# Performance work log

Hardware: AMD Instinct MI355X
Metric: run time of the kernel (lower is better)

The kernel has to match this reference:

```python
import jax, jax.numpy as jnp
import numpy as np

DIM = 192
HEADS = 4


def setup_inputs() -> dict:
    key = jax.random.key(0)
    ks = jax.random.split(key, 6)
    b, h, w = 8, 128, 128
    return {
        "x": jax.random.normal(ks[0], (b, DIM, h, w), jnp.float32),
        "svp_fea": jax.random.normal(ks[1], (b, 3, h, w), jnp.float32),
        "qkv_w": jax.random.normal(ks[2], (3 * DIM, DIM), jnp.float32) * 0.02,
        "dw_w": jax.random.normal(ks[3], (3 * DIM, 1, 3, 3), jnp.float32) * 0.02,
        "svp_w": jax.random.normal(ks[4], (3 * HEADS, 3), jnp.float32) * 0.02,
        "proj_w": jax.random.normal(ks[5], (DIM, DIM + 3 * HEADS), jnp.float32) * 0.02,
        "temperature": jnp.ones((HEADS, 1, 1), jnp.float32),
    }


def _l2norm(t):
    # F.normalize(t, dim=-1): divide by max(||t||_2, eps)
    return t / jnp.maximum(jnp.linalg.norm(t, axis=-1, keepdims=True), 1e-12)


def reference(x, svp_fea, qkv_w, dw_w, svp_w, proj_w, temperature):
    b, c, h, w = x.shape
    heads = temperature.shape[0]
    # 1x1 conv (dim -> 3*dim), then 3x3 depthwise conv (groups = 3*dim)
    qkv = jnp.einsum('bchw,oc->bohw', x, qkv_w)
    qkv = jax.lax.conv_general_dilated(
        qkv, dw_w, window_strides=(1, 1), padding=((1, 1), (1, 1)),
        dimension_numbers=('NCHW', 'OIHW', 'NCHW'), feature_group_count=3 * c)
    # 1x1 conv on illumination prior: 3 -> 3*heads
    svp_q = jnp.einsum('bchw,oc->bohw', svp_fea, svp_w)
    q, k, v = jnp.split(qkv, 3, axis=1)
    ch = c // heads
    hw = h * w
    q = _l2norm(q.reshape(b, heads, ch, hw))
    k = _l2norm(k.reshape(b, heads, ch, hw))
    v = v.reshape(b, heads, ch, hw)
    sq = _l2norm(svp_q.reshape(b, heads, 3, hw))
    q = jnp.concatenate([q, sq], axis=2)            # [b, head, ch+3, hw]
    logits = jnp.einsum('bhcn,bhdn->bhcd', q, k) * temperature[None]
    attn = jax.nn.softmax(logits, axis=-1)          # softmax over channel dim d
    out = jnp.einsum('bhcd,bhdn->bhcn', attn, v)    # [b, head, ch+3, hw]
    out = out.reshape(b, heads * (ch + 3), h, w)
    return jnp.einsum('bchw,oc->bohw', out, proj_w)
```

## Files before the change

### kernel.cpp

```cpp
#include <hip/hip_runtime.h>
#include <hip/hip_bf16.h>
#include <math.h>

#define BB   8
#define CCH  192
#define OCN  576
#define HWD  128
#define HWN  16384
#define NH   4
#define CHD  48
#define C51  51
#define GSZ  (C51*48)

typedef __hip_bfloat16 bf16;
typedef __attribute__((ext_vector_type(8))) short short8;
typedef __attribute__((ext_vector_type(4))) float f32x4;

__device__ __forceinline__ float bfbits2f(unsigned int u16) {
  union { unsigned int i; float f; } v; v.i = u16 << 16; return v.f;
}
__device__ __forceinline__ unsigned short f2bfbits(float f) {
  __hip_bfloat16 h = __float2bfloat16(f);
  return *(unsigned short*)&h;
}
__device__ __forceinline__ void stage16(const void* g, void* l) {
  __builtin_amdgcn_global_load_lds(
      (const __attribute__((address_space(1))) void*)g,
      (__attribute__((address_space(3))) void*)l, 16, 0, 0);
}

__global__ __launch_bounds__(256) void k_svp(
    const float* __restrict__ svp_fea, const float* __restrict__ svp_w,
    float* __restrict__ svp_q, float* __restrict__ ssq_svp_p)
{
  __shared__ float lsw[4][12];
  const int b = blockIdx.y;
  const int t = threadIdx.x;
  const int n = blockIdx.x * 256 + t;
  const int wave = t >> 6;
  const float* fb = svp_fea + (size_t)b * 3 * HWN;
  const float f0 = fb[n], f1 = fb[HWN + n], f2 = fb[2 * HWN + n];
  float* ob = svp_q + (size_t)b * 12 * HWN + n;
  #pragma unroll
  for (int r = 0; r < 12; ++r) {
    float o = svp_w[r*3]*f0 + svp_w[r*3+1]*f1 + svp_w[r*3+2]*f2;
    ob[(size_t)r * HWN] = o;
    float v = o * o;
    #pragma unroll
    for (int off = 32; off >= 1; off >>= 1) v += __shfl_down(v, off, 64);
    if ((t & 63) == 0) lsw[wave][r] = v;
  }
  __syncthreads();
  if (t < 12) {
    float s = lsw[0][t] + lsw[1][t] + lsw[2][t] + lsw[3][t];
    ssq_svp_p[((size_t)b * 12 + t) * 64 + blockIdx.x] = s;
  }
}

__global__ __launch_bounds__(256) void k_castw(
    const float* __restrict__ w, unsigned short* __restrict__ wb)
{
  const int i = (blockIdx.x * 256 + threadIdx.x) * 4;
  float4 v = *(const float4*)(w + i);
  union { uint2 u; unsigned short s[4]; } pk;
  pk.s[0] = f2bfbits(v.x); pk.s[1] = f2bfbits(v.y);
  pk.s[2] = f2bfbits(v.z); pk.s[3] = f2bfbits(v.w);
  *(uint2*)(wb + i) = pk.u;
}

__global__ __launch_bounds__(256) void k_gemm(
    const float* __restrict__ x, const unsigned short* __restrict__ wb,
    unsigned short* __restrict__ qkv1)
{
  __shared__ unsigned short Xs[64 * CCH];
  __shared__ unsigned short Ws[96 * CCH];
  const int b = blockIdx.y;
  const int n0 = blockIdx.x * 64;
  const int t = threadIdx.x;
  const int lane = t & 63, wave = t >> 6;
  const int wm = wave >> 1, wn = wave & 1;
  const int lq = lane >> 4, lr = lane & 15;

  const float* xb = x + (size_t)b * CCH * HWN + n0;
  #pragma unroll
  for (int rr = 0; rr < 6; ++rr) {
    int idx = rr * 256 + t;
    int cp = idx >> 4, nq = idx & 15;
    int c0 = cp * 2;
    float4 v0 = *(const float4*)(xb + (size_t)c0 * HWN + nq * 4);
    float4 v1 = *(const float4*)(xb + (size_t)(c0 + 1) * HWN + nq * 4);
    int g = c0 >> 3, co = c0 & 7;
    float a0[4] = {v0.x, v0.y, v0.z, v0.w};
    float a1[4] = {v1.x, v1.y, v1.z, v1.w};
    #pragma unroll
    for (int j = 0; j < 4; ++j) {
      int n = nq * 4 + j;
      int gs = (g & ~7) | ((g & 7) ^ (n & 7) ^ ((n >> 3) & 7));
      unsigned int pk = (unsigned int)f2bfbits(a0[j])
                      | ((unsigned int)f2bfbits(a1[j]) << 16);
      *(unsigned int*)&Xs[n * CCH + gs * 8 + co] = pk;
    }
  }

  for (int mc = 0; mc < 6; ++mc) {
    const unsigned short* wsrc = wb + (size_t)mc * 96 * CCH;
    #pragma unroll
    for (int i = 0; i < 9; ++i) {
      int chunk = wave * 9 + i;
      int d = chunk * 64 + lane;
      int row = d / 24, kg = d % 24;
      int skg = (kg & ~7) | ((kg & 7) ^ (row & 7));
      stage16(wsrc + (size_t)row * CCH + skg * 8, &Ws[0] + chunk * 512);
    }
    asm volatile("s_waitcnt vmcnt(0)" ::: "memory");
    __syncthreads();

    f32x4 acc[3][2];
    #pragma unroll
    for (int mf = 0; mf < 3; ++mf)
      #pragma unroll
      for (int nf = 0; nf < 2; ++nf) acc[mf][nf] = (f32x4)0.f;

    #pragma unroll
    for (int ks = 0; ks < 6; ++ks) {
      const int gk = ks * 4 + lq;
      short8 a[3], bb[2];
      #pragma unroll
      for (int mf = 0; mf < 3; ++mf) {
        int r = wm * 48 + mf * 16 + lr;
        int sg = (gk & ~7) | ((gk & 7) ^ (r & 7));
        a[mf] = *(const short8*)&Ws[r * CCH + sg * 8];
      }
      #pragma unroll
      for (int nf = 0; nf < 2; ++nf) {
        int r = wn * 32 + nf * 16 + lr;
        int sg = (gk & ~7) | ((gk & 7) ^ (r & 7) ^ ((r >> 3) & 7));
        bb[nf] = *(const short8*)&Xs[r * CCH + sg * 8];
      }
      #pragma unroll
      for (int mf = 0; mf < 3; ++mf)
        #pragma unroll
        for (int nf = 0; nf < 2; ++nf)
          acc[mf][nf] = __builtin_amdgcn_mfma_f32_16x16x32_bf16(
              a[mf], bb[nf], acc[mf][nf], 0, 0, 0);
    }

    unsigned short* ob = qkv1 + ((size_t)b * OCN + mc * 96 + wm * 48) * HWN
                         + n0 + wn * 32;
    #pragma unroll
    for (int mf = 0; mf < 3; ++mf)
      #pragma unroll
      for (int nf = 0; nf < 2; ++nf)
        #pragma unroll
        for (int r = 0; r < 4; ++r) {
          int m = mf * 16 + lq * 4 + r;
          int n = nf * 16 + lr;
          ob[(size_t)m * HWN + n] = f2bfbits(acc[mf][nf][r]);
        }
    __syncthreads();
  }
}

__global__ __launch_bounds__(256) void k_dw(
    const unsigned short* __restrict__ qkv1, const float* __restrict__ dw_w,
    unsigned short* __restrict__ qkv, float* __restrict__ ssq_qk_p)
{
  __shared__ float lsw[4];
  const int b = blockIdx.z, c = blockIdx.y, slab = blockIdx.x;
  const int t = threadIdx.x;
  const int cg = t & 15, rg = t >> 4;
  const int y0 = slab * 32 + rg * 2;
  const unsigned short* src = qkv1 + ((size_t)b * OCN + c) * HWN;
  float w[9];
  #pragma unroll
  for (int i = 0; i < 9; ++i) w[i] = dw_w[c * 9 + i];

  float rows[4][10];
  #pragma unroll
  for (int j = 0; j < 4; ++j) {
    int gr = y0 - 1 + j;
    uint4 B = make_uint4(0u, 0u, 0u, 0u);
    unsigned int Al = 0; unsigned int Cv = 0;
    if ((unsigned)gr < 128u) {
      const unsigned short* rp = src + (size_t)gr * HWD;
      B = *(const uint4*)(rp + cg * 8);
      if (cg > 0)  Al = *(const unsigned int*)(rp + cg * 8 - 2);
      if (cg < 15) Cv = (unsigned int)rp[cg * 8 + 8];
    }
    rows[j][0] = bfbits2f(Al >> 16);
    unsigned int ub[4] = {B.x, B.y, B.z, B.w};
    #pragma unroll
    for (int q = 0; q < 4; ++q) {
      rows[j][1 + 2*q] = bfbits2f(ub[q] & 0xffffu);
      rows[j][2 + 2*q] = bfbits2f(ub[q] >> 16);
    }
    rows[j][9] = bfbits2f(Cv);
  }

  unsigned short* dst = qkv + ((size_t)b * OCN + c) * HWN;
  float ssq = 0.f;
  #pragma unroll
  for (int e = 0; e < 2; ++e) {
    float acc[8];
    #pragma unroll
    for (int i = 0; i < 8; ++i) acc[i] = 0.f;
    #pragma unroll
    for (int j = 0; j < 3; ++j) {
      const float* vr = rows[e + j];
      #pragma unroll
      for (int i = 0; i < 8; ++i)
        acc[i] += w[j*3]*vr[i] + w[j*3+1]*vr[i+1] + w[j*3+2]*vr[i+2];
    }
    union { uint4 u; unsigned short s[8]; } pk;
    #pragma unroll
    for (int i = 0; i < 8; ++i) pk.s[i] = f2bfbits(acc[i]);
    *(uint4*)(dst + (size_t)(y0 + e) * HWD + cg * 8) = pk.u;
    if (c < 384) {
      #pragma unroll
      for (int i = 0; i < 8; ++i) {
        float rv = bfbits2f(pk.s[i]);
        ssq += rv * rv;
      }
    }
  }
  if (c < 384) {
    #pragma unroll
    for (int off = 32; off >= 1; off >>= 1) ssq += __shfl_down(ssq, off, 64);
    if ((t & 63) == 0) lsw[t >> 6] = ssq;
  }
  __syncthreads();
  if (c < 384 && t == 0)
    ssq_qk_p[(((size_t)b * 384 + c) << 2) | slab] =
        lsw[0] + lsw[1] + lsw[2] + lsw[3];
}

__global__ __launch_bounds__(256) void k_gram(
    const unsigned short* __restrict__ qkv, const float* __restrict__ svp_q,
    float* __restrict__ Gp)
{
  __shared__ float Gs[C51 * 50];
  const int chunk = blockIdx.x, h = blockIdx.y, b = blockIdx.z;
  const int t = threadIdx.x;
  const int lane = t & 63, wave = t >> 6;
  const int lq = lane >> 4, lr = lane & 15;
  const unsigned short* qb = qkv + ((size_t)b*OCN + h*CHD)*HWN;
  const unsigned short* kb = qkv + ((size_t)b*OCN + 192 + h*CHD)*HWN;
  const float* sb = svp_q + ((size_t)b*12 + h*3)*HWN;

  for (int idx = t; idx < C51*50; idx += 256) Gs[idx] = 0.f;

  f32x4 acc[3][3], sacc[3];
  #pragma unroll
  for (int mf = 0; mf < 3; ++mf)
    #pragma unroll
    for (int nf = 0; nf < 3; ++nf) acc[mf][nf] = (f32x4)0.f;
  #pragma unroll
  for (int nf = 0; nf < 3; ++nf) sacc[nf] = (f32x4)0.f;

  const int nbase = chunk * 1024 + wave * 256;
  #pragma unroll 4
  for (int ks = 0; ks < 8; ++ks) {
    const int n = nbase + ks * 32 + lq * 8;
    short8 a[3], bb[3];
    #pragma unroll
    for (int mf = 0; mf < 3; ++mf)
      a[mf] = *(const short8*)&qb[(size_t)(mf*16 + lr)*HWN + n];
    #pragma unroll
    for (int nf = 0; nf < 3; ++nf)
      bb[nf] = *(const short8*)&kb[(size_t)(nf*16 + lr)*HWN + n];
    union { short8 s8; unsigned short us[8]; } sv;
    #pragma unroll
    for (int i = 0; i < 8; ++i) sv.us[i] = 0;
    if (lr < 3) {
      const float* sp = sb + (size_t)lr*HWN + n;
      float4 v0 = *(const float4*)sp, v1 = *(const float4*)(sp + 4);
      sv.us[0] = f2bfbits(v0.x); sv.us[1] = f2bfbits(v0.y);
      sv.us[2] = f2bfbits(v0.z); sv.us[3] = f2bfbits(v0.w);
      sv.us[4] = f2bfbits(v1.x); sv.us[5] = f2bfbits(v1.y);
      sv.us[6] = f2bfbits(v1.z); sv.us[7] = f2bfbits(v1.w);
    }
    #pragma unroll
    for (int mf = 0; mf < 3; ++mf)
      #pragma unroll
      for (int nf = 0; nf < 3; ++nf)
        acc[mf][nf] = __builtin_amdgcn_mfma_f32_16x16x32_bf16(
            a[mf], bb[nf], acc[mf][nf], 0, 0, 0);
    #pragma unroll
    for (int nf = 0; nf < 3; ++nf)
      sacc[nf] = __builtin_amdgcn_mfma_f32_16x16x32_bf16(
          sv.s8, bb[nf], sacc[nf], 0, 0, 0);
  }

  __syncthreads();
  for (int w = 0; w < 4; ++w) {
    if (wave == w) {
      #pragma unroll
      for (int mf = 0; mf < 3; ++mf)
        #pragma unroll
        for (int nf = 0; nf < 3; ++nf)
          #pragma unroll
          for (int r = 0; r < 4; ++r)
            Gs[(mf*16 + lq*4 + r)*50 + nf*16 + lr] += acc[mf][nf][r];
      if (lq == 0) {
        #pragma unroll
        for (int nf = 0; nf < 3; ++nf)
          #pragma unroll
          for (int r = 0; r < 3; ++r)
            Gs[(48 + r)*50 + nf*16 + lr] += sacc[nf][r];
      }
    }
    __syncthreads();
  }
  float* Gout = Gp + ((size_t)((b*NH + h) * 16 + chunk)) * GSZ;
  for (int idx = t; idx < GSZ; idx += 256) {
    int row = idx / 48, col = idx - row * 48;
    Gout[idx] = Gs[row*50 + col];
  }
}

__global__ __launch_bounds__(256) void k_attn_fold(
    const float* __restrict__ Gp, const float* __restrict__ ssq_qk_p,
    const float* __restrict__ ssq_svp_p, const float* __restrict__ temperature,
    const float* __restrict__ proj_w, unsigned short* __restrict__ W2bf)
{
  __shared__ float A[GSZ];
  __shared__ float qinv[C51];
  __shared__ float kinv[48];
  const int h = blockIdx.x, b = blockIdx.y;
  const int t = threadIdx.x;
  const float* Gb = Gp + ((size_t)(b*NH + h) * 16) * GSZ;
  if (t < 48) {
    const float* p = ssq_qk_p + (((size_t)b * 384 + 192 + h*48 + t) << 2);
    kinv[t] = 1.f / fmaxf(sqrtf(p[0] + p[1] + p[2] + p[3]), 1e-12f);
  }
  if (t >= 64 && t < 64 + C51) {
    int c = t - 64;
    float ss;
    if (c < 48) {
      const float* p = ssq_qk_p + (((size_t)b * 384 + h*48 + c) << 2);
      ss = p[0] + p[1] + p[2] + p[3];
    } else {
      const float* p = ssq_svp_p + ((size_t)b * 12 + h*3 + (c - 48)) * 64;
      float s0 = 0.f, s1 = 0.f, s2 = 0.f, s3 = 0.f;
      #pragma unroll
      for (int i = 0; i < 16; ++i) {
        float4 v = *(const float4*)(p + i * 4);
        s0 += v.x; s1 += v.y; s2 += v.z; s3 += v.w;
      }
      ss = (s0 + s1) + (s2 + s3);
    }
    qinv[c] = 1.f / fmaxf(sqrtf(ss), 1e-12f);
  }
  for (int idx = t; idx < GSZ; idx += 256) {
    float s = 0.f;
    #pragma unroll
    for (int c = 0; c < 16; ++c) s += Gb[(size_t)c * GSZ + idx];
    A[idx] = s;
  }
  __syncthreads();
  const float temp = temperature[h];
  if (t < C51) {
    float row[48];
    float m = -1e30f;
    const float qi = qinv[t] * temp;
    #pragma unroll
    for (int d = 0; d < 48; ++d) {
      float l = A[t*48 + d] * qi * kinv[d];
      row[d] = l; m = fmaxf(m, l);
    }
    float s = 0.f;
    #pragma unroll
    for (int d = 0; d < 48; ++d) { row[d] = expf(row[d] - m); s += row[d]; }
    const float inv = 1.f / s;
    #pragma unroll
    for (int d = 0; d < 48; ++d) A[t*48 + d] = row[d] * inv;
  }
  __syncthreads();
  for (int idx = t; idx < 192*48; idx += 256) {
    int o = idx / 48, d = idx - o*48;
    const float* pw = proj_w + o*204 + C51*h;
    float s = 0.f;
    #pragma unroll
    for (int c = 0; c < C51; ++c) s += pw[c] * A[c*48 + d];
    W2bf[((size_t)b*CCH + o)*CCH + h*48 + d] = f2bfbits(s);
  }
}

__global__ __launch_bounds__(256) void k_out(
    const unsigned short* __restrict__ qkv, const unsigned short* __restrict__ w2b,
    float* __restrict__ out)
{
  __shared__ unsigned short Vs[64 * CCH];
  __shared__ unsigned short Ws[96 * CCH];
  const int b = blockIdx.y;
  const int n0 = blockIdx.x * 64;
  const int t = threadIdx.x;
  const int lane = t & 63, wave = t >> 6;
  const int wm = wave >> 1, wn = wave & 1;
  const int lq = lane >> 4, lr = lane & 15;

  const unsigned short* vb = qkv + ((size_t)b * OCN + 384) * HWN + n0;
  #pragma unroll
  for (int rr = 0; rr < 3; ++rr) {
    int idx = rr * 256 + t;
    int cp = idx >> 3, nq = idx & 7;
    int c0 = cp * 2;
    uint4 v0 = *(const uint4*)(vb + (size_t)c0 * HWN + nq * 8);
    uint4 v1 = *(const uint4*)(vb + (size_t)(c0 + 1) * HWN + nq * 8);
    union { uint4 u; unsigned short s[8]; } p0, p1;
    p0.u = v0; p1.u = v1;
    int g = c0 >> 3, co = c0 & 7;
    #pragma unroll
    for (int j = 0; j < 8; ++j) {
      int n = nq * 8 + j;
      int gs = (g & ~7) | ((g & 7) ^ (n & 7) ^ ((n >> 3) & 7));
      unsigned int pk = (unsigned int)p0.s[j] | ((unsigned int)p1.s[j] << 16);
      *(unsigned int*)&Vs[n * CCH + gs * 8 + co] = pk;
    }
  }

  for (int mc = 0; mc < 2; ++mc) {
    const unsigned short* wsrc = w2b + ((size_t)b * CCH + mc * 96) * CCH;
    #pragma unroll
    for (int i = 0; i < 9; ++i) {
      int chunk = wave * 9 + i;
      int d = chunk * 64 + lane;
      int row = d / 24, kg = d % 24;
      int skg = (kg & ~7) | ((kg & 7) ^ (row & 7));
      stage16(wsrc + (size_t)row * CCH + skg * 8, &Ws[0] + chunk * 512);
    }
    asm volatile("s_waitcnt vmcnt(0)" ::: "memory");
    __syncthreads();

    f32x4 acc[3][2];
    #pragma unroll
    for (int mf = 0; mf < 3; ++mf)
      #pragma unroll
      for (int nf = 0; nf < 2; ++nf) acc[mf][nf] = (f32x4)0.f;

    #pragma unroll
    for (int ks = 0; ks < 6; ++ks) {
      const int gk = ks * 4 + lq;
      short8 a[3], bb[2];
      #pragma unroll
      for (int mf = 0; mf < 3; ++mf) {
        int r = wm * 48 + mf * 16 + lr;
        int sg = (gk & ~7) | ((gk & 7) ^ (r & 7));
        a[mf] = *(const short8*)&Ws[r * CCH + sg * 8];
      }
      #pragma unroll
      for (int nf = 0; nf < 2; ++nf) {
        int r = wn * 32 + nf * 16 + lr;
        int sg = (gk & ~7) | ((gk & 7) ^ (r & 7) ^ ((r >> 3) & 7));
        bb[nf] = *(const short8*)&Vs[r * CCH + sg * 8];
      }
      #pragma unroll
      for (int mf = 0; mf < 3; ++mf)
        #pragma unroll
        for (int nf = 0; nf < 2; ++nf)
          acc[mf][nf] = __builtin_amdgcn_mfma_f32_16x16x32_bf16(
              a[mf], bb[nf], acc[mf][nf], 0, 0, 0);
    }

    float* ob = out + ((size_t)b * CCH + mc * 96 + wm * 48) * HWN + n0 + wn * 32;
    #pragma unroll
    for (int mf = 0; mf < 3; ++mf)
      #pragma unroll
      for (int nf = 0; nf < 2; ++nf)
        #pragma unroll
        for (int r = 0; r < 4; ++r) {
          int m = mf * 16 + lq * 4 + r;
          int n = nf * 16 + lr;
          ob[(size_t)m * HWN + n] = acc[mf][nf][r];
        }
    __syncthreads();
  }
}

extern "C" void kernel_launch(void* const* d_in, const int* in_sizes, int n_in,
                              void* d_out, int out_size, void* d_ws, size_t ws_size,
                              hipStream_t stream)
{
  const float* x       = (const float*)d_in[0];
  const float* svp_fea = (const float*)d_in[1];
  const float* qkv_w   = (const float*)d_in[2];
  const float* dw_w    = (const float*)d_in[3];
  const float* svp_w   = (const float*)d_in[4];
  const float* proj_w  = (const float*)d_in[5];
  const float* temp    = (const float*)d_in[6];
  float* outp = (float*)d_out;

  char* ws = (char*)d_ws;
  const size_t off_qkv1   = 0;
  const size_t off_qkv    = off_qkv1  + (size_t)BB*OCN*HWN*2;
  const size_t off_wb     = off_qkv   + (size_t)BB*OCN*HWN*2;
  const size_t off_svpq   = off_wb    + (size_t)OCN*CCH*2;
  const size_t off_ssqqk  = off_svpq  + (size_t)BB*12*HWN*4;
  const size_t off_ssqsvp = off_ssqqk + (size_t)BB*384*4*4;
  const size_t off_Gp     = off_ssqsvp+ (size_t)BB*12*64*4;
  const size_t off_W2     = off_Gp    + (size_t)BB*NH*16*GSZ*4;

  unsigned short* qkv1  = (unsigned short*)(ws + off_qkv1);
  bf16*  qkv     = (bf16*)(ws + off_qkv);
  unsigned short* wb    = (unsigned short*)(ws + off_wb);
  float* svp_q   = (float*)(ws + off_svpq);
  float* ssq_qk_p  = (float*)(ws + off_ssqqk);
  float* ssq_svp_p = (float*)(ws + off_ssqsvp);
  float* Gp      = (float*)(ws + off_Gp);
  unsigned short* W2bf  = (unsigned short*)(ws + off_W2);

  k_castw    <<<dim3(108),         256, 0, stream>>>(qkv_w, wb);
  k_svp      <<<dim3(64, BB),      256, 0, stream>>>(svp_fea, svp_w, svp_q, ssq_svp_p);
  k_gemm     <<<dim3(256, BB),     256, 0, stream>>>(x, wb, qkv1);
  k_dw       <<<dim3(4, OCN, BB),  256, 0, stream>>>(qkv1, dw_w, (unsigned short*)qkv, ssq_qk_p);
  k_gram     <<<dim3(16, NH, BB),  256, 0, stream>>>((const unsigned short*)qkv, svp_q, Gp);
  k_attn_fold<<<dim3(NH, BB),      256, 0, stream>>>(Gp, ssq_qk_p, ssq_svp_p, temp, proj_w, W2bf);
  k_out      <<<dim3(256, BB),     256, 0, stream>>>((const unsigned short*)qkv, W2bf, outp);
}
```

Before: 282.7 us.

## Load weight fragments directly from global into registers and hoist B fragments

In both the qkv GEMM and the output GEMM, the weight tile is no longer staged through LDS with global_load_lds. Each wave now reads its A fragments straight from global memory into registers. The activation fragments are read from LDS once into registers before the output-channel loop, which removes the per-iteration barriers and LDS traffic and halves LDS use per block, so occupancy can rise. In exchange, weight rows are re-read from global or L2 by every wave with less coalescing, and register pressure goes up from holding 18 A and 12 B fragments.

```diff
diff --git a/kernel.cpp b/kernel.cpp
--- a/kernel.cpp
+++ b/kernel.cpp
@@ -23,11 +23,6 @@
   __hip_bfloat16 h = __float2bfloat16(f);
   return *(unsigned short*)&h;
 }
-__device__ __forceinline__ void stage16(const void* g, void* l) {
-  __builtin_amdgcn_global_load_lds(
-      (const __attribute__((address_space(1))) void*)g,
-      (__attribute__((address_space(3))) void*)l, 16, 0, 0);
-}
 
 __global__ __launch_bounds__(256) void k_svp(
     const float* __restrict__ svp_fea, const float* __restrict__ svp_w,
@@ -73,7 +68,6 @@
     unsigned short* __restrict__ qkv1)
 {
   __shared__ unsigned short Xs[64 * CCH];
-  __shared__ unsigned short Ws[96 * CCH];
   const int b = blockIdx.y;
   const int n0 = blockIdx.x * 64;
   const int t = threadIdx.x;
@@ -101,20 +95,29 @@
       *(unsigned int*)&Xs[n * CCH + gs * 8 + co] = pk;
     }
   }
+  __syncthreads();
+
+  short8 bfr[2][6];
+  #pragma unroll
+  for (int nf = 0; nf < 2; ++nf) {
+    int r = wn * 32 + nf * 16 + lr;
+    #pragma unroll
+    for (int ks = 0; ks < 6; ++ks) {
+      int gk = ks * 4 + lq;
+      int sg = (gk & ~7) | ((gk & 7) ^ (r & 7) ^ ((r >> 3) & 7));
+      bfr[nf][ks] = *(const short8*)&Xs[r * CCH + sg * 8];
+    }
+  }
 
   for (int mc = 0; mc < 6; ++mc) {
-    const unsigned short* wsrc = wb + (size_t)mc * 96 * CCH;
-    #pragma unroll
-    for (int i = 0; i < 9; ++i) {
-      int chunk = wave * 9 + i;
-      int d = chunk * 64 + lane;
-      int row = d / 24, kg = d % 24;
-      int skg = (kg & ~7) | ((kg & 7) ^ (row & 7));
-      stage16(wsrc + (size_t)row * CCH + skg * 8, &Ws[0] + chunk * 512);
-    }
-    asm volatile("s_waitcnt vmcnt(0)" ::: "memory");
-    __syncthreads();
-
+    const unsigned short* wsrc = wb + ((size_t)mc * 96 + wm * 48 + lr) * CCH;
+    short8 a[3][6];
+    #pragma unroll
+    for (int mf = 0; mf < 3; ++mf)
+      #pragma unroll
+      for (int ks = 0; ks < 6; ++ks)
+        a[mf][ks] = *(const short8*)(wsrc + (size_t)mf * 16 * CCH
+                                     + (ks * 4 + lq) * 8);
     f32x4 acc[3][2];
     #pragma unroll
     for (int mf = 0; mf < 3; ++mf)
@@ -122,28 +125,13 @@
       for (int nf = 0; nf < 2; ++nf) acc[mf][nf] = (f32x4)0.f;
 
     #pragma unroll
-    for (int ks = 0; ks < 6; ++ks) {
-      const int gk = ks * 4 + lq;
-      short8 a[3], bb[2];
-      #pragma unroll
-      for (int mf = 0; mf < 3; ++mf) {
-        int r = wm * 48 + mf * 16 + lr;
-        int sg = (gk & ~7) | ((gk & 7) ^ (r & 7));
-        a[mf] = *(const short8*)&Ws[r * CCH + sg * 8];
-      }
-      #pragma unroll
-      for (int nf = 0; nf < 2; ++nf) {
-        int r = wn * 32 + nf * 16 + lr;
-        int sg = (gk & ~7) | ((gk & 7) ^ (r & 7) ^ ((r >> 3) & 7));
-        bb[nf] = *(const short8*)&Xs[r * CCH + sg * 8];
-      }
+    for (int ks = 0; ks < 6; ++ks)
       #pragma unroll
       for (int mf = 0; mf < 3; ++mf)
         #pragma unroll
         for (int nf = 0; nf < 2; ++nf)
           acc[mf][nf] = __builtin_amdgcn_mfma_f32_16x16x32_bf16(
-              a[mf], bb[nf], acc[mf][nf], 0, 0, 0);
-    }
+              a[mf][ks], bfr[nf][ks], acc[mf][nf], 0, 0, 0);
 
     unsigned short* ob = qkv1 + ((size_t)b * OCN + mc * 96 + wm * 48) * HWN
                          + n0 + wn * 32;
@@ -157,7 +145,6 @@
           int n = nf * 16 + lr;
           ob[(size_t)m * HWN + n] = f2bfbits(acc[mf][nf][r]);
         }
-    __syncthreads();
   }
 }
 
@@ -391,7 +378,6 @@
     float* __restrict__ out)
 {
   __shared__ unsigned short Vs[64 * CCH];
-  __shared__ unsigned short Ws[96 * CCH];
   const int b = blockIdx.y;
   const int n0 = blockIdx.x * 64;
   const int t = threadIdx.x;
@@ -418,20 +404,29 @@
       *(unsigned int*)&Vs[n * CCH + gs * 8 + co] = pk;
     }
   }
+  __syncthreads();
+
+  short8 bfr[2][6];
+  #pragma unroll
+  for (int nf = 0; nf < 2; ++nf) {
+    int r = wn * 32 + nf * 16 + lr;
+    #pragma unroll
+    for (int ks = 0; ks < 6; ++ks) {
+      int gk = ks * 4 + lq;
+      int sg = (gk & ~7) | ((gk & 7) ^ (r & 7) ^ ((r >> 3) & 7));
+      bfr[nf][ks] = *(const short8*)&Vs[r * CCH + sg * 8];
+    }
+  }
 
   for (int mc = 0; mc < 2; ++mc) {
-    const unsigned short* wsrc = w2b + ((size_t)b * CCH + mc * 96) * CCH;
-    #pragma unroll
-    for (int i = 0; i < 9; ++i) {
-      int chunk = wave * 9 + i;
-      int d = chunk * 64 + lane;
-      int row = d / 24, kg = d % 24;
-      int skg = (kg & ~7) | ((kg & 7) ^ (row & 7));
-      stage16(wsrc + (size_t)row * CCH + skg * 8, &Ws[0] + chunk * 512);
-    }
-    asm volatile("s_waitcnt vmcnt(0)" ::: "memory");
-    __syncthreads();
-
+    const unsigned short* wsrc = w2b + ((size_t)b * CCH + mc * 96 + wm * 48 + lr) * CCH;
+    short8 a[3][6];
+    #pragma unroll
+    for (int mf = 0; mf < 3; ++mf)
+      #pragma unroll
+      for (int ks = 0; ks < 6; ++ks)
+        a[mf][ks] = *(const short8*)(wsrc + (size_t)mf * 16 * CCH
+                                     + (ks * 4 + lq) * 8);
     f32x4 acc[3][2];
     #pragma unroll
     for (int mf = 0; mf < 3; ++mf)
@@ -439,28 +434,13 @@
       for (int nf = 0; nf < 2; ++nf) acc[mf][nf] = (f32x4)0.f;
 
     #pragma unroll
-    for (int ks = 0; ks < 6; ++ks) {
-      const int gk = ks * 4 + lq;
-      short8 a[3], bb[2];
-      #pragma unroll
-      for (int mf = 0; mf < 3; ++mf) {
-        int r = wm * 48 + mf * 16 + lr;
-        int sg = (gk & ~7) | ((gk & 7) ^ (r & 7));
-        a[mf] = *(const short8*)&Ws[r * CCH + sg * 8];
-      }
-      #pragma unroll
-      for (int nf = 0; nf < 2; ++nf) {
-        int r = wn * 32 + nf * 16 + lr;
-        int sg = (gk & ~7) | ((gk & 7) ^ (r & 7) ^ ((r >> 3) & 7));
-        bb[nf] = *(const short8*)&Vs[r * CCH + sg * 8];
-      }
+    for (int ks = 0; ks < 6; ++ks)
       #pragma unroll
       for (int mf = 0; mf < 3; ++mf)
         #pragma unroll
         for (int nf = 0; nf < 2; ++nf)
           acc[mf][nf] = __builtin_amdgcn_mfma_f32_16x16x32_bf16(
-              a[mf], bb[nf], acc[mf][nf], 0, 0, 0);
-    }
+              a[mf][ks], bfr[nf][ks], acc[mf][nf], 0, 0, 0);
 
     float* ob = out + ((size_t)b * CCH + mc * 96 + wm * 48) * HWN + n0 + wn * 32;
     #pragma unroll
@@ -473,7 +453,6 @@
           int n = nf * 16 + lr;
           ob[(size_t)m * HWN + n] = acc[mf][nf][r];
         }
-    __syncthreads();
   }
 }
 
```

After: 362.4 us. 1.28x slower.

## Double-buffer weight tiles and keep B fragments in registers in GEMM kernels

Applied to the files above, without the earlier changes.

Both the qkv 1x1-conv GEMM and the output projection GEMM now stream the weight matrix in 32-row chunks through a two-slot LDS buffer. The next chunk is prefetched while the current one is multiplied, and the input (X or V) MFMA fragments are loaded from LDS into registers once instead of on every chunk. The aim is to hide global weight-load latency behind MFMA work, cut repeated LDS reads, and lower LDS footprint so more blocks fit per CU. In exchange there are more loop iterations and barriers, and each wave issues fewer MFMAs per chunk, which may limit instruction-level parallelism.

```diff
diff --git a/kernel.cpp b/kernel.cpp
--- a/kernel.cpp
+++ b/kernel.cpp
@@ -73,13 +73,22 @@
     unsigned short* __restrict__ qkv1)
 {
   __shared__ unsigned short Xs[64 * CCH];
-  __shared__ unsigned short Ws[96 * CCH];
+  __shared__ unsigned short Wd[2][32 * CCH];
   const int b = blockIdx.y;
   const int n0 = blockIdx.x * 64;
   const int t = threadIdx.x;
   const int lane = t & 63, wave = t >> 6;
   const int wm = wave >> 1, wn = wave & 1;
   const int lq = lane >> 4, lr = lane & 15;
+
+  #pragma unroll
+  for (int i = 0; i < 3; ++i) {
+    int chunk = wave * 3 + i;
+    int d = chunk * 64 + lane;
+    int row = d / 24, kg = d % 24;
+    int skg = (kg & ~7) | ((kg & 7) ^ (row & 7));
+    stage16(wb + (size_t)row * CCH + skg * 8, &Wd[0][0] + chunk * 512);
+  }
 
   const float* xb = x + (size_t)b * CCH * HWN + n0;
   #pragma unroll
@@ -101,63 +110,60 @@
       *(unsigned int*)&Xs[n * CCH + gs * 8 + co] = pk;
     }
   }
-
-  for (int mc = 0; mc < 6; ++mc) {
-    const unsigned short* wsrc = wb + (size_t)mc * 96 * CCH;
-    #pragma unroll
-    for (int i = 0; i < 9; ++i) {
-      int chunk = wave * 9 + i;
-      int d = chunk * 64 + lane;
-      int row = d / 24, kg = d % 24;
-      int skg = (kg & ~7) | ((kg & 7) ^ (row & 7));
-      stage16(wsrc + (size_t)row * CCH + skg * 8, &Ws[0] + chunk * 512);
-    }
-    asm volatile("s_waitcnt vmcnt(0)" ::: "memory");
-    __syncthreads();
-
-    f32x4 acc[3][2];
-    #pragma unroll
-    for (int mf = 0; mf < 3; ++mf)
-      #pragma unroll
-      for (int nf = 0; nf < 2; ++nf) acc[mf][nf] = (f32x4)0.f;
-
+  __syncthreads();
+
+  short8 bfr[2][6];
+  #pragma unroll
+  for (int nf = 0; nf < 2; ++nf) {
+    int r = wn * 32 + nf * 16 + lr;
+    #pragma unroll
+    for (int ks = 0; ks < 6; ++ks) {
+      int gk = ks * 4 + lq;
+      int sg = (gk & ~7) | ((gk & 7) ^ (r & 7) ^ ((r >> 3) & 7));
+      bfr[nf][ks] = *(const short8*)&Xs[r * CCH + sg * 8];
+    }
+  }
+
+  for (int mc = 0; mc < 18; ++mc) {
+    if (mc + 1 < 18) {
+      const unsigned short* wsrc = wb + (size_t)(mc + 1) * 32 * CCH;
+      unsigned short* nb = &Wd[(mc + 1) & 1][0];
+      #pragma unroll
+      for (int i = 0; i < 3; ++i) {
+        int chunk = wave * 3 + i;
+        int d = chunk * 64 + lane;
+        int row = d / 24, kg = d % 24;
+        int skg = (kg & ~7) | ((kg & 7) ^ (row & 7));
+        stage16(wsrc + (size_t)row * CCH + skg * 8, nb + chunk * 512);
+      }
+      asm volatile("s_waitcnt vmcnt(3)" ::: "memory");
+    } else {
+      asm volatile("s_waitcnt vmcnt(0)" ::: "memory");
+    }
+    __builtin_amdgcn_s_barrier();
+    asm volatile("" ::: "memory");
+
+    const unsigned short* wbuf = &Wd[mc & 1][0];
+    f32x4 acc0 = (f32x4)0.f, acc1 = (f32x4)0.f;
     #pragma unroll
     for (int ks = 0; ks < 6; ++ks) {
       const int gk = ks * 4 + lq;
-      short8 a[3], bb[2];
-      #pragma unroll
-      for (int mf = 0; mf < 3; ++mf) {
-        int r = wm * 48 + mf * 16 + lr;
-        int sg = (gk & ~7) | ((gk & 7) ^ (r & 7));
-        a[mf] = *(const short8*)&Ws[r * CCH + sg * 8];
-      }
-      #pragma unroll
-      for (int nf = 0; nf < 2; ++nf) {
-        int r = wn * 32 + nf * 16 + lr;
-        int sg = (gk & ~7) | ((gk & 7) ^ (r & 7) ^ ((r >> 3) & 7));
-        bb[nf] = *(const short8*)&Xs[r * CCH + sg * 8];
-      }
-      #pragma unroll
-      for (int mf = 0; mf < 3; ++mf)
-        #pragma unroll
-        for (int nf = 0; nf < 2; ++nf)
-          acc[mf][nf] = __builtin_amdgcn_mfma_f32_16x16x32_bf16(
-              a[mf], bb[nf], acc[mf][nf], 0, 0, 0);
-    }
-
-    unsigned short* ob = qkv1 + ((size_t)b * OCN + mc * 96 + wm * 48) * HWN
+      int r = wm * 16 + lr;
+      int sg = (gk & ~7) | ((gk & 7) ^ (r & 7));
+      short8 a = *(const short8*)&wbuf[r * CCH + sg * 8];
+      acc0 = __builtin_amdgcn_mfma_f32_16x16x32_bf16(a, bfr[0][ks], acc0, 0, 0, 0);
+      acc1 = __builtin_amdgcn_mfma_f32_16x16x32_bf16(a, bfr[1][ks], acc1, 0, 0, 0);
+    }
+
+    unsigned short* ob = qkv1 + ((size_t)b * OCN + mc * 32 + wm * 16) * HWN
                          + n0 + wn * 32;
     #pragma unroll
-    for (int mf = 0; mf < 3; ++mf)
-      #pragma unroll
-      for (int nf = 0; nf < 2; ++nf)
-        #pragma unroll
-        for (int r = 0; r < 4; ++r) {
-          int m = mf * 16 + lq * 4 + r;
-          int n = nf * 16 + lr;
-          ob[(size_t)m * HWN + n] = f2bfbits(acc[mf][nf][r]);
-        }
-    __syncthreads();
+    for (int r = 0; r < 4; ++r) {
+      ob[(size_t)(lq * 4 + r) * HWN + lr]      = f2bfbits(acc0[r]);
+      ob[(size_t)(lq * 4 + r) * HWN + 16 + lr] = f2bfbits(acc1[r]);
+    }
+    asm volatile("" ::: "memory");
+    __builtin_amdgcn_s_barrier();
   }
 }
 
@@ -391,13 +397,23 @@
     float* __restrict__ out)
 {
   __shared__ unsigned short Vs[64 * CCH];
-  __shared__ unsigned short Ws[96 * CCH];
+  __shared__ unsigned short Wd[2][32 * CCH];
   const int b = blockIdx.y;
   const int n0 = blockIdx.x * 64;
   const int t = threadIdx.x;
   const int lane = t & 63, wave = t >> 6;
   const int wm = wave >> 1, wn = wave & 1;
   const int lq = lane >> 4, lr = lane & 15;
+
+  const unsigned short* w2base = w2b + (size_t)b * CCH * CCH;
+  #pragma unroll
+  for (int i = 0; i < 3; ++i) {
+    int chunk = wave * 3 + i;
+    int d = chunk * 64 + lane;
+    int row = d / 24, kg = d % 24;
+    int skg = (kg & ~7) | ((kg & 7) ^ (row & 7));
+    stage16(w2base + (size_t)row * CCH + skg * 8, &Wd[0][0] + chunk * 512);
+  }
 
   const unsigned short* vb = qkv + ((size_t)b * OCN + 384) * HWN + n0;
   #pragma unroll
@@ -418,62 +434,59 @@
       *(unsigned int*)&Vs[n * CCH + gs * 8 + co] = pk;
     }
   }
-
-  for (int mc = 0; mc < 2; ++mc) {
-    const unsigned short* wsrc = w2b + ((size_t)b * CCH + mc * 96) * CCH;
-    #pragma unroll
-    for (int i = 0; i < 9; ++i) {
-      int chunk = wave * 9 + i;
-      int d = chunk * 64 + lane;
-      int row = d / 24, kg = d % 24;
-      int skg = (kg & ~7) | ((kg & 7) ^ (row & 7));
-      stage16(wsrc + (size_t)row * CCH + skg * 8, &Ws[0] + chunk * 512);
-    }
-    asm volatile("s_waitcnt vmcnt(0)" ::: "memory");
-    __syncthreads();
-
-    f32x4 acc[3][2];
-    #pragma unroll
-    for (int mf = 0; mf < 3; ++mf)
-      #pragma unroll
-      for (int nf = 0; nf < 2; ++nf) acc[mf][nf] = (f32x4)0.f;
-
+  __syncthreads();
+
+  short8 bfr[2][6];
+  #pragma unroll
+  for (int nf = 0; nf < 2; ++nf) {
+    int r = wn * 32 + nf * 16 + lr;
+    #pragma unroll
+    for (int ks = 0; ks < 6; ++ks) {
+      int gk = ks * 4 + lq;
+      int sg = (gk & ~7) | ((gk & 7) ^ (r & 7) ^ ((r >> 3) & 7));
+      bfr[nf][ks] = *(const short8*)&Vs[r * CCH + sg * 8];
+    }
+  }
+
+  for (int mc = 0; mc < 6; ++mc) {
+    if (mc + 1 < 6) {
+      const unsigned short* wsrc = w2base + (size_t)(mc + 1) * 32 * CCH;
+      unsigned short* nb = &Wd[(mc + 1) & 1][0];
+      #pragma unroll
+      for (int i = 0; i < 3; ++i) {
+        int chunk = wave * 3 + i;
+        int d = chunk * 64 + lane;
+        int row = d / 24, kg = d % 24;
+        int skg = (kg & ~7) | ((kg & 7) ^ (row & 7));
+        stage16(wsrc + (size_t)row * CCH + skg * 8, nb + chunk * 512);
+      }
+      asm volatile("s_waitcnt vmcnt(3)" ::: "memory");
+    } else {
+      asm volatile("s_waitcnt vmcnt(0)" ::: "memory");
+    }
+    __builtin_amdgcn_s_barrier();
+    asm volatile("" ::: "memory");
+
+    const unsigned short* wbuf = &Wd[mc & 1][0];
+    f32x4 acc0 = (f32x4)0.f, acc1 = (f32x4)0.f;
     #pragma unroll
     for (int ks = 0; ks < 6; ++ks) {
       const int gk = ks * 4 + lq;
-      short8 a[3], bb[2];
-      #pragma unroll
-      for (int mf = 0; mf < 3; ++mf) {
-        int r = wm * 48 + mf * 16 + lr;
-        int sg = (gk & ~7) | ((gk & 7) ^ (r & 7));
-        a[mf] = *(const short8*)&Ws[r * CCH + sg * 8];
-      }
-      #pragma unroll
-      for (int nf = 0; nf < 2; ++nf) {
-        int r = wn * 32 + nf * 16 + lr;
-        int sg = (gk & ~7) | ((gk & 7) ^ (r & 7) ^ ((r >> 3) & 7));
-        bb[nf] = *(const short8*)&Vs[r * CCH + sg * 8];
-      }
-      #pragma unroll
-      for (int mf = 0; mf < 3; ++mf)
-        #pragma unroll
-        for (int nf = 0; nf < 2; ++nf)
-          acc[mf][nf] = __builtin_amdgcn_mfma_f32_16x16x32_bf16(
-              a[mf], bb[nf], acc[mf][nf], 0, 0, 0);
-    }
-
-    float* ob = out + ((size_t)b * CCH + mc * 96 + wm * 48) * HWN + n0 + wn * 32;
-    #pragma unroll
-    for (int mf = 0; mf < 3; ++mf)
-      #pragma unroll
-      for (int nf = 0; nf < 2; ++nf)
-        #pragma unroll
-        for (int r = 0; r < 4; ++r) {
-          int m = mf * 16 + lq * 4 + r;
-          int n = nf * 16 + lr;
-          ob[(size_t)m * HWN + n] = acc[mf][nf][r];
-        }
-    __syncthreads();
+      int r = wm * 16 + lr;
+      int sg = (gk & ~7) | ((gk & 7) ^ (r & 7));
+      short8 a = *(const short8*)&wbuf[r * CCH + sg * 8];
+      acc0 = __builtin_amdgcn_mfma_f32_16x16x32_bf16(a, bfr[0][ks], acc0, 0, 0, 0);
+      acc1 = __builtin_amdgcn_mfma_f32_16x16x32_bf16(a, bfr[1][ks], acc1, 0, 0, 0);
+    }
+
+    float* ob = out + ((size_t)b * CCH + mc * 32 + wm * 16) * HWN + n0 + wn * 32;
+    #pragma unroll
+    for (int r = 0; r < 4; ++r) {
+      ob[(size_t)(lq * 4 + r) * HWN + lr]      = acc0[r];
+      ob[(size_t)(lq * 4 + r) * HWN + 16 + lr] = acc1[r];
+    }
+    asm volatile("" ::: "memory");
+    __builtin_amdgcn_s_barrier();
   }
 }
 
```

New measurement: 279.5 us. Within noise of the previous version (-1.1%).
